# Kernel tuning notes

Hardware: AMD Instinct MI355X
Metric: run time of the kernel (lower is better)

The kernel has to match this reference:

```python
import jax, jax.numpy as jnp
import numpy as np

XY, Zs, V = 32, 16, 10000
N = XY * XY * Zs            # 16384 states
B, T, L = 32, 64, 16
# neighbor offsets from transition_log_p: (x,y,z) -> x + XY*(y + XY*z)
OFFS = np.array([0, 1, -1, XY, -XY, XY * XY, 2 * XY * XY], dtype=np.int64)
NBR = (np.arange(N)[:, None] - OFFS[None, :]) % N   # [N,7] source-state index per neighbor


def setup_inputs() -> dict:
    key = jax.random.key(0)
    k1, k2, k3, k4 = jax.random.split(key, 4)
    return {
        "stories_tensor": jax.random.randint(k1, (B, T, L), 0, V),
        "story_length": T,
        "length": L,
        "trans_unnorm": jax.random.normal(k2, (N, 7), dtype=jnp.float32),
        "emis_unnorm": jax.random.normal(k3, (N, V), dtype=jnp.float32),
        "prior_unnorm": jax.random.normal(k4, (N,), dtype=jnp.float32),
    }


def reference(stories_tensor, story_length, length, trans_unnorm, emis_unnorm, prior_unnorm):
    logT = jax.nn.log_softmax(trans_unnorm, axis=-1)     # [N,7]
    logE = jax.nn.log_softmax(emis_unnorm, axis=1)       # [N,V]
    logpi = jax.nn.log_softmax(prior_unnorm, axis=0)     # [N]
    nbr = jnp.asarray(NBR)                               # [N,7]

    def emit(tokens):                                    # [B,L] -> [B,N]
        # emission_log_p: logE[:, tokens] -> [N,B,L], sum over words, transpose
        return jnp.swapaxes(logE[:, tokens].sum(-1), 0, 1)

    scores0 = emit(stories_tensor[:, 0]) + logpi[None, :]   # [B,N]

    def step(scores, tokens):
        em = emit(tokens)                                # [B,N]
        prev = scores[:, nbr]                            # [B,N,7] gather of prior alpha
        new = em + jax.scipy.special.logsumexp(logT[None, :, :] + prev, axis=-1)
        return new, None

    seq = jnp.swapaxes(stories_tensor, 0, 1)[1:]         # [T-1,B,L]
    scores, _ = jax.lax.scan(step, scores0, seq)
    return jax.scipy.special.logsumexp(scores, axis=-1)  # [B]
```

## Files before the change

kernel.cpp:

```cpp
#include <hip/hip_runtime.h>
#include <stdint.h>

#define XY 32
#define ZS 16
#define NST 16384
#define NMASK 16383
#define VOC 10000
#define BB 32
#define TT 64
#define LL 16
#define HALO 32
#define BUFSZ (NST + 2 * HALO)

#define LOG2E 1.4426950408889634f
#define LN2F  0.6931471805599453f

__device__ __forceinline__ float fexp2(float x) {
#if __has_builtin(__builtin_amdgcn_exp2f)
  return __builtin_amdgcn_exp2f(x);
#else
  return exp2f(x);
#endif
}
__device__ __forceinline__ float flog2(float x) {
#if __has_builtin(__builtin_amdgcn_logf)
  return __builtin_amdgcn_logf(x);
#else
  return log2f(x);
#endif
}

__device__ __forceinline__ float waveMax(float v) {
  #pragma unroll
  for (int o = 32; o >= 1; o >>= 1) v = fmaxf(v, __shfl_xor(v, o, 64));
  return v;
}
__device__ __forceinline__ float waveSum(float v) {
  #pragma unroll
  for (int o = 32; o >= 1; o >>= 1) v += __shfl_xor(v, o, 64);
  return v;
}

__global__ __launch_bounds__(256) void tok_conv(const int* __restrict__ st,
                                                unsigned short* __restrict__ tok16) {
  int i = blockIdx.x * 256 + threadIdx.x;
  if (i >= BB * TT * LL) return;
  int l = i & 15;
  int tb = i >> 4;
  int b = tb & 31;
  int t = tb >> 5;
  tok16[i] = (unsigned short)st[b * (TT * LL) + t * LL + l];
}

__global__ __launch_bounds__(256) void prep_trans(const float* __restrict__ tr,
                                                  float* __restrict__ Tn) {
  int n = blockIdx.x * 256 + threadIdx.x;
  if (n >= NST) return;
  float v[7];
  float m = -3.4e38f;
  #pragma unroll
  for (int k = 0; k < 7; ++k) { v[k] = tr[n * 7 + k]; m = fmaxf(m, v[k]); }
  float s = 0.f;
  #pragma unroll
  for (int k = 0; k < 7; ++k) { v[k] = fexp2((v[k] - m) * LOG2E); s += v[k]; }
  float inv = 1.0f / s;
  #pragma unroll
  for (int k = 0; k < 7; ++k) Tn[n * 8 + k] = v[k] * inv;
  Tn[n * 8 + 7] = 0.f;
}

__global__ __launch_bounds__(256) void lse_prior(const float* __restrict__ prior,
                                                 float* __restrict__ lse_p) {
  int tid = threadIdx.x;
  __shared__ float sred[8];
  float lmax = -3.4e38f;
  for (int n = tid; n < NST; n += 256) lmax = fmaxf(lmax, prior[n]);
  float wm = waveMax(lmax);
  if ((tid & 63) == 0) sred[tid >> 6] = wm;
  __syncthreads();
  float bm = fmaxf(fmaxf(sred[0], sred[1]), fmaxf(sred[2], sred[3]));
  float ls = 0.f;
  for (int n = tid; n < NST; n += 256) ls += fexp2((prior[n] - bm) * LOG2E);
  float ws = waveSum(ls);
  if ((tid & 63) == 0) sred[4 + (tid >> 6)] = ws;
  __syncthreads();
  if (tid == 0)
    lse_p[0] = bm + flog2(sred[4] + sred[5] + sred[6] + sred[7]) * LN2F;
}

__global__ __launch_bounds__(256) void emis_kernel(const float* __restrict__ emis,
                                                   const unsigned short* __restrict__ tok16,
                                                   float* __restrict__ em) {
  const int n = blockIdx.x;
  const int tid = threadIdx.x;
  __shared__ float row[VOC];
  __shared__ float sred[8];

  const float4* rp = (const float4*)(emis + (size_t)n * VOC);
  float4 regs[10];
  float lmax = -3.4e38f;
  #pragma unroll
  for (int it = 0; it < 10; ++it) {
    int i = tid + it * 256;
    if (i < VOC / 4) {
      float4 v = rp[i];
      regs[it] = v;
      ((float4*)row)[i] = v;
      lmax = fmaxf(lmax, fmaxf(fmaxf(v.x, v.y), fmaxf(v.z, v.w)));
    }
  }
  float wm = waveMax(lmax);
  if ((tid & 63) == 0) sred[tid >> 6] = wm;
  __syncthreads();
  float bm = fmaxf(fmaxf(sred[0], sred[1]), fmaxf(sred[2], sred[3]));

  float ls = 0.f;
  #pragma unroll
  for (int it = 0; it < 10; ++it) {
    int i = tid + it * 256;
    if (i < VOC / 4) {
      float4 v = regs[it];
      ls += fexp2((v.x - bm) * LOG2E);
      ls += fexp2((v.y - bm) * LOG2E);
      ls += fexp2((v.z - bm) * LOG2E);
      ls += fexp2((v.w - bm) * LOG2E);
    }
  }
  float wsum = waveSum(ls);
  if ((tid & 63) == 0) sred[4 + (tid >> 6)] = wsum;
  __syncthreads();
  float lse = bm + flog2(sred[4] + sred[5] + sred[6] + sred[7]) * LN2F;
  float sub = (float)LL * lse;

  for (int i = tid; i < TT * BB; i += 256) {
    const uint4* tp = (const uint4*)(tok16 + (size_t)i * 16);
    uint4 w0 = tp[0];
    uint4 w1 = tp[1];
    float s = row[w0.x & 0xFFFF] + row[w0.x >> 16]
            + row[w0.y & 0xFFFF] + row[w0.y >> 16]
            + row[w0.z & 0xFFFF] + row[w0.z >> 16]
            + row[w0.w & 0xFFFF] + row[w0.w >> 16]
            + row[w1.x & 0xFFFF] + row[w1.x >> 16]
            + row[w1.y & 0xFFFF] + row[w1.y >> 16]
            + row[w1.z & 0xFFFF] + row[w1.z >> 16]
            + row[w1.w & 0xFFFF] + row[w1.w >> 16];
    em[(size_t)n * (TT * BB) + i] = (s - sub) * LOG2E;
  }
}

__global__ __launch_bounds__(256) void transpose_em(const float* __restrict__ em,
                                                    float* __restrict__ em2) {
  __shared__ float tile[64][65];
  const int i0 = blockIdx.x * 64;
  const int n0 = blockIdx.y * 64;
  const int tx = threadIdx.x & 63;
  const int ty = threadIdx.x >> 6;
  #pragma unroll
  for (int r = 0; r < 16; ++r) {
    int nr = ty + 4 * r;
    tile[nr][tx] = em[(size_t)(n0 + nr) * (TT * BB) + i0 + tx];
  }
  __syncthreads();
  #pragma unroll
  for (int r = 0; r < 16; ++r) {
    int ir = ty + 4 * r;
    em2[(size_t)(i0 + ir) * NST + n0 + tx] = tile[tx][ir];
  }
}

__global__ __launch_bounds__(1024) void recursion_kernel(const float* __restrict__ em2,
                                                         const float* __restrict__ Tn8,
                                                         const float* __restrict__ prior,
                                                         const float* __restrict__ lse_p,
                                                         float* __restrict__ out) {
  extern __shared__ float lds[];
  float* buf0 = lds;
  float* buf1 = lds + BUFSZ;
  const int b = blockIdx.x;
  const int tid = threadIdx.x;

  {
    const float* e0 = em2 + ((size_t)b << 14);
    #pragma unroll
    for (int s = 0; s < 16; ++s) {
      int n = tid + (s << 10);
      float v = e0[n] + prior[n] * LOG2E;
      buf0[HALO + n] = v;
      if (n < HALO) buf0[HALO + NST + n] = v;
      if (n >= NST - HALO) buf0[n - (NST - HALO)] = v;
    }
  }
  __syncthreads();

  for (int t = 1; t < TT; ++t) {
    const float* prev = (t & 1) ? buf0 : buf1;
    float* cur = (t & 1) ? buf1 : buf0;
    const float* e = em2 + ((size_t)(t * BB + b) << 14);
    float pm1 = prev[HALO + ((tid - 1024) & NMASK)];
    float pm2 = prev[HALO + ((tid - 2048) & NMASK)];
    #pragma unroll
    for (int s = 0; s < 16; ++s) {
      int n = tid + (s << 10);
      float p0 = prev[HALO + n];
      float a1 = prev[HALO + n - 1];
      float a2 = prev[HALO + n + 1];
      float a3 = prev[HALO + n - 32];
      float a4 = prev[HALO + n + 32];
      float p5 = pm1;
      float p6 = pm2;
      const float4* tp = (const float4*)(Tn8 + ((size_t)n << 3));
      float4 ta = tp[0];
      float4 tb = tp[1];
      float m = fmaxf(fmaxf(fmaxf(p0, a1), fmaxf(a2, a3)),
                      fmaxf(fmaxf(a4, p5), p6));
      float ssum = ta.x * fexp2(p0 - m) + ta.y * fexp2(a1 - m)
                 + ta.z * fexp2(a2 - m) + ta.w * fexp2(a3 - m)
                 + tb.x * fexp2(a4 - m) + tb.y * fexp2(p5 - m)
                 + tb.z * fexp2(p6 - m);
      float v = e[n] + m + flog2(ssum);
      cur[HALO + n] = v;
      if (n < HALO) cur[HALO + NST + n] = v;
      if (n >= NST - HALO) cur[n - (NST - HALO)] = v;
      pm2 = pm1;
      pm1 = p0;
    }
    __syncthreads();
  }

  float lm = -3.4e38f;
  #pragma unroll
  for (int s = 0; s < 16; ++s)
    lm = fmaxf(lm, buf1[HALO + tid + (s << 10)]);
  lm = waveMax(lm);
  if ((tid & 63) == 0) buf0[tid >> 6] = lm;
  __syncthreads();
  float bm = buf0[0];
  #pragma unroll
  for (int k = 1; k < 16; ++k) bm = fmaxf(bm, buf0[k]);
  float ls = 0.f;
  #pragma unroll
  for (int s = 0; s < 16; ++s)
    ls += fexp2(buf1[HALO + tid + (s << 10)] - bm);
  ls = waveSum(ls);
  if ((tid & 63) == 0) buf0[16 + (tid >> 6)] = ls;
  __syncthreads();
  if (tid == 0) {
    float s = 0.f;
    #pragma unroll
    for (int k = 0; k < 16; ++k) s += buf0[16 + k];
    out[b] = LN2F * (bm + flog2(s)) - lse_p[0];
  }
}

extern "C" void kernel_launch(void* const* d_in, const int* in_sizes, int n_in,
                              void* d_out, int out_size, void* d_ws, size_t ws_size,
                              hipStream_t stream) {
  const int* stories  = (const int*)d_in[0];
  const float* trans  = (const float*)d_in[3];
  const float* emis   = (const float*)d_in[4];
  const float* prior  = (const float*)d_in[5];
  float* out = (float*)d_out;

  char* ws = (char*)d_ws;
  float* em  = (float*)ws;
  float* em2 = em + (size_t)NST * TT * BB;
  float* Tn  = em2 + (size_t)NST * TT * BB;
  unsigned short* tok16 = (unsigned short*)(Tn + (size_t)NST * 8);
  float* lse_p = (float*)(tok16 + (size_t)BB * TT * LL);

  tok_conv<<<(BB * TT * LL + 255) / 256, 256, 0, stream>>>(stories, tok16);
  prep_trans<<<NST / 256, 256, 0, stream>>>(trans, Tn);
  lse_prior<<<1, 256, 0, stream>>>(prior, lse_p);
  emis_kernel<<<NST, 256, 0, stream>>>(emis, tok16, em);
  transpose_em<<<dim3(TT * BB / 64, NST / 64), 256, 0, stream>>>(em, em2);

  size_t dynlds = (size_t)2 * BUFSZ * sizeof(float);
  hipFuncSetAttribute((const void*)recursion_kernel,
                      hipFuncAttributeMaxDynamicSharedMemorySize, (int)dynlds);
  recursion_kernel<<<BB, 1024, dynlds, stream>>>(em2, Tn, prior, lse_p, out);
}
```

Measured before the change: 1.488 ms.

## Split HMM recursion across 8 chunk blocks per batch with neighbor flag sync

The forward recursion used to run as one 1024-thread block per batch element, which occupies only 32 CUs. It now runs on 256 blocks, each owning a 2048-state chunk of one batch. Each step exchanges state through global double buffers and waits only on per-block flags of the two neighboring chunks, and a final cross-chunk log-sum-exp merges per-chunk partials. Transition weights move to a planar layout cached in LDS. In exchange each step pays a global write, a staged reload of neighbor halos and spin-wait latency, and the scheme depends on all 256 blocks being co-resident to avoid deadlock.

```diff
diff --git a/kernel.cpp b/kernel.cpp
--- a/kernel.cpp
+++ b/kernel.cpp
@@ -9,8 +9,11 @@
 #define BB 32
 #define TT 64
 #define LL 16
-#define HALO 32
-#define BUFSZ (NST + 2 * HALO)
+
+#define NCHUNK 8
+#define CSZ 2048
+#define STAGE_N (CSZ + CSZ + 32)
+#define STAGE_PAD 4160
 
 #define LOG2E 1.4426950408889634f
 #define LN2F  0.6931471805599453f
@@ -53,7 +56,7 @@
 }
 
 __global__ __launch_bounds__(256) void prep_trans(const float* __restrict__ tr,
-                                                  float* __restrict__ Tn) {
+                                                  float* __restrict__ TnG) {
   int n = blockIdx.x * 256 + threadIdx.x;
   if (n >= NST) return;
   float v[7];
@@ -65,8 +68,7 @@
   for (int k = 0; k < 7; ++k) { v[k] = fexp2((v[k] - m) * LOG2E); s += v[k]; }
   float inv = 1.0f / s;
   #pragma unroll
-  for (int k = 0; k < 7; ++k) Tn[n * 8 + k] = v[k] * inv;
-  Tn[n * 8 + 7] = 0.f;
+  for (int k = 0; k < 7; ++k) TnG[k * NST + n] = v[k] * inv;
 }
 
 __global__ __launch_bounds__(256) void lse_prior(const float* __restrict__ prior,
@@ -86,6 +88,10 @@
   __syncthreads();
   if (tid == 0)
     lse_p[0] = bm + flog2(sred[4] + sred[5] + sred[6] + sred[7]) * LN2F;
+}
+
+__global__ __launch_bounds__(64) void init_flags(int* flags) {
+  flags[threadIdx.x + blockIdx.x * 64] = -1;
 }
 
 __global__ __launch_bounds__(256) void emis_kernel(const float* __restrict__ emis,
@@ -168,87 +174,143 @@
   }
 }
 
-__global__ __launch_bounds__(1024) void recursion_kernel(const float* __restrict__ em2,
-                                                         const float* __restrict__ Tn8,
-                                                         const float* __restrict__ prior,
-                                                         const float* __restrict__ lse_p,
-                                                         float* __restrict__ out) {
+__global__ __launch_bounds__(256) void recursion_kernel(
+    const float* __restrict__ em2,
+    const float* __restrict__ TnG,
+    const float* __restrict__ prior,
+    const float* __restrict__ lse_p,
+    float* __restrict__ S0,
+    float* __restrict__ S1,
+    int* flags,
+    float2* partials,
+    float* __restrict__ out) {
   extern __shared__ float lds[];
-  float* buf0 = lds;
-  float* buf1 = lds + BUFSZ;
-  const int b = blockIdx.x;
+  float* stage = lds;
+  float* TnT   = lds + STAGE_PAD;
+  float* red   = TnT + 7 * CSZ;
+
+  const int bid = blockIdx.x;
+  const int b = bid & 31;
+  const int c = bid >> 5;
+  const int c0 = c * CSZ;
   const int tid = threadIdx.x;
-
-  {
-    const float* e0 = em2 + ((size_t)b << 14);
+  const int lbid = (((c + NCHUNK - 1) & (NCHUNK - 1)) << 5) | b;
+  const int rbid = (((c + 1) & (NCHUNK - 1)) << 5) | b;
+
+  #pragma unroll
+  for (int j = 0; j < 7; ++j) {
+    const float4* src = (const float4*)(TnG + (size_t)j * NST + c0);
+    float4* dst = (float4*)(TnT + j * CSZ);
+    for (int i = tid; i < CSZ / 4; i += 256) dst[i] = src[i];
+  }
+
+  #pragma unroll
+  for (int k = 0; k < 8; ++k) {
+    int s = tid + (k << 8);
+    int n = c0 + s;
+    S0[(size_t)b * NST + n] = em2[(size_t)b * NST + n] + prior[n] * LOG2E;
+  }
+  __syncthreads();
+  if (tid == 0)
+    __hip_atomic_store(&flags[bid], 0, __ATOMIC_RELEASE, __HIP_MEMORY_SCOPE_AGENT);
+
+  float vcur[8];
+  for (int t = 1; t < TT; ++t) {
+    const float* __restrict__ Sprev = (t & 1) ? S0 : S1;
+    float* __restrict__ Scur = (t & 1) ? S1 : S0;
+
+    if (tid == 0) {
+      while (__hip_atomic_load(&flags[lbid], __ATOMIC_RELAXED,
+                               __HIP_MEMORY_SCOPE_AGENT) < t - 1)
+        __builtin_amdgcn_s_sleep(1);
+      while (__hip_atomic_load(&flags[rbid], __ATOMIC_RELAXED,
+                               __HIP_MEMORY_SCOPE_AGENT) < t - 1)
+        __builtin_amdgcn_s_sleep(1);
+    }
+    __syncthreads();
+    __builtin_amdgcn_fence(__ATOMIC_ACQUIRE, "agent");
+
+    {
+      const int base = (c0 - CSZ) & NMASK;
+      const float* sp = Sprev + (size_t)b * NST;
+      for (int i = tid; i < STAGE_N / 4; i += 256) {
+        int idx = (base + 4 * i) & NMASK;
+        *(float4*)(stage + 4 * i) = *(const float4*)(sp + idx);
+      }
+    }
+    __syncthreads();
+
+    const float* __restrict__ e = em2 + (size_t)(t * BB + b) * NST + c0;
     #pragma unroll
-    for (int s = 0; s < 16; ++s) {
-      int n = tid + (s << 10);
-      float v = e0[n] + prior[n] * LOG2E;
-      buf0[HALO + n] = v;
-      if (n < HALO) buf0[HALO + NST + n] = v;
-      if (n >= NST - HALO) buf0[n - (NST - HALO)] = v;
-    }
-  }
-  __syncthreads();
-
-  for (int t = 1; t < TT; ++t) {
-    const float* prev = (t & 1) ? buf0 : buf1;
-    float* cur = (t & 1) ? buf1 : buf0;
-    const float* e = em2 + ((size_t)(t * BB + b) << 14);
-    float pm1 = prev[HALO + ((tid - 1024) & NMASK)];
-    float pm2 = prev[HALO + ((tid - 2048) & NMASK)];
-    #pragma unroll
-    for (int s = 0; s < 16; ++s) {
-      int n = tid + (s << 10);
-      float p0 = prev[HALO + n];
-      float a1 = prev[HALO + n - 1];
-      float a2 = prev[HALO + n + 1];
-      float a3 = prev[HALO + n - 32];
-      float a4 = prev[HALO + n + 32];
-      float p5 = pm1;
-      float p6 = pm2;
-      const float4* tp = (const float4*)(Tn8 + ((size_t)n << 3));
-      float4 ta = tp[0];
-      float4 tb = tp[1];
+    for (int k = 0; k < 8; ++k) {
+      int s = tid + (k << 8);
+      float p0 = stage[CSZ + s];
+      float a1 = stage[CSZ + s - 1];
+      float a2 = stage[CSZ + s + 1];
+      float a3 = stage[CSZ + s - 32];
+      float a4 = stage[CSZ + s + 32];
+      float p5 = stage[CSZ + s - 1024];
+      float p6 = stage[s];
+      float t0 = TnT[0 * CSZ + s], t1 = TnT[1 * CSZ + s], t2 = TnT[2 * CSZ + s],
+            t3 = TnT[3 * CSZ + s], t4 = TnT[4 * CSZ + s], t5 = TnT[5 * CSZ + s],
+            t6 = TnT[6 * CSZ + s];
       float m = fmaxf(fmaxf(fmaxf(p0, a1), fmaxf(a2, a3)),
                       fmaxf(fmaxf(a4, p5), p6));
-      float ssum = ta.x * fexp2(p0 - m) + ta.y * fexp2(a1 - m)
-                 + ta.z * fexp2(a2 - m) + ta.w * fexp2(a3 - m)
-                 + tb.x * fexp2(a4 - m) + tb.y * fexp2(p5 - m)
-                 + tb.z * fexp2(p6 - m);
-      float v = e[n] + m + flog2(ssum);
-      cur[HALO + n] = v;
-      if (n < HALO) cur[HALO + NST + n] = v;
-      if (n >= NST - HALO) cur[n - (NST - HALO)] = v;
-      pm2 = pm1;
-      pm1 = p0;
-    }
-    __syncthreads();
-  }
-
-  float lm = -3.4e38f;
-  #pragma unroll
-  for (int s = 0; s < 16; ++s)
-    lm = fmaxf(lm, buf1[HALO + tid + (s << 10)]);
-  lm = waveMax(lm);
-  if ((tid & 63) == 0) buf0[tid >> 6] = lm;
-  __syncthreads();
-  float bm = buf0[0];
-  #pragma unroll
-  for (int k = 1; k < 16; ++k) bm = fmaxf(bm, buf0[k]);
-  float ls = 0.f;
-  #pragma unroll
-  for (int s = 0; s < 16; ++s)
-    ls += fexp2(buf1[HALO + tid + (s << 10)] - bm);
-  ls = waveSum(ls);
-  if ((tid & 63) == 0) buf0[16 + (tid >> 6)] = ls;
+      float ssum = t0 * fexp2(p0 - m) + t1 * fexp2(a1 - m)
+                 + t2 * fexp2(a2 - m) + t3 * fexp2(a3 - m)
+                 + t4 * fexp2(a4 - m) + t5 * fexp2(p5 - m)
+                 + t6 * fexp2(p6 - m);
+      vcur[k] = e[s] + m + flog2(ssum);
+    }
+
+    if (t < TT - 1) {
+      #pragma unroll
+      for (int k = 0; k < 8; ++k)
+        Scur[(size_t)b * NST + c0 + tid + (k << 8)] = vcur[k];
+      __syncthreads();
+      if (tid == 0)
+        __hip_atomic_store(&flags[bid], t, __ATOMIC_RELEASE,
+                           __HIP_MEMORY_SCOPE_AGENT);
+    }
+  }
+
+  float mr = vcur[0];
+  #pragma unroll
+  for (int k = 1; k < 8; ++k) mr = fmaxf(mr, vcur[k]);
+  mr = waveMax(mr);
+  if ((tid & 63) == 0) red[tid >> 6] = mr;
+  __syncthreads();
+  float M = fmaxf(fmaxf(red[0], red[1]), fmaxf(red[2], red[3]));
+  float sr = 0.f;
+  #pragma unroll
+  for (int k = 0; k < 8; ++k) sr += fexp2(vcur[k] - M);
+  sr = waveSum(sr);
+  if ((tid & 63) == 0) red[4 + (tid >> 6)] = sr;
   __syncthreads();
   if (tid == 0) {
-    float s = 0.f;
+    partials[bid] = make_float2(M, red[4] + red[5] + red[6] + red[7]);
+    __hip_atomic_store(&flags[bid], TT - 1, __ATOMIC_RELEASE,
+                       __HIP_MEMORY_SCOPE_AGENT);
+  }
+
+  if (c == 0 && tid == 0) {
     #pragma unroll
-    for (int k = 0; k < 16; ++k) s += buf0[16 + k];
-    out[b] = LN2F * (bm + flog2(s)) - lse_p[0];
+    for (int cc = 1; cc < NCHUNK; ++cc) {
+      int fb = (cc << 5) | b;
+      while (__hip_atomic_load(&flags[fb], __ATOMIC_RELAXED,
+                               __HIP_MEMORY_SCOPE_AGENT) < TT - 1)
+        __builtin_amdgcn_s_sleep(1);
+    }
+    __builtin_amdgcn_fence(__ATOMIC_ACQUIRE, "agent");
+    float Mg = -3.4e38f, Sg = 0.f;
+    #pragma unroll
+    for (int cc = 0; cc < NCHUNK; ++cc) {
+      float2 p = partials[(cc << 5) | b];
+      float nm = fmaxf(Mg, p.x);
+      Sg = Sg * fexp2(Mg - nm) + p.y * fexp2(p.x - nm);
+      Mg = nm;
+    }
+    out[b] = LN2F * (Mg + flog2(Sg)) - lse_p[0];
   }
 }
 
@@ -264,18 +326,24 @@
   char* ws = (char*)d_ws;
   float* em  = (float*)ws;
   float* em2 = em + (size_t)NST * TT * BB;
-  float* Tn  = em2 + (size_t)NST * TT * BB;
-  unsigned short* tok16 = (unsigned short*)(Tn + (size_t)NST * 8);
+  float* S0  = em2 + (size_t)NST * TT * BB;
+  float* S1  = S0 + (size_t)BB * NST;
+  float* TnG = S1 + (size_t)BB * NST;
+  float2* partials = (float2*)(TnG + (size_t)7 * NST);
+  int* flags = (int*)(partials + 256);
+  unsigned short* tok16 = (unsigned short*)(flags + 256);
   float* lse_p = (float*)(tok16 + (size_t)BB * TT * LL);
 
+  init_flags<<<4, 64, 0, stream>>>(flags);
   tok_conv<<<(BB * TT * LL + 255) / 256, 256, 0, stream>>>(stories, tok16);
-  prep_trans<<<NST / 256, 256, 0, stream>>>(trans, Tn);
+  prep_trans<<<NST / 256, 256, 0, stream>>>(trans, TnG);
   lse_prior<<<1, 256, 0, stream>>>(prior, lse_p);
   emis_kernel<<<NST, 256, 0, stream>>>(emis, tok16, em);
   transpose_em<<<dim3(TT * BB / 64, NST / 64), 256, 0, stream>>>(em, em2);
 
-  size_t dynlds = (size_t)2 * BUFSZ * sizeof(float);
+  size_t dynlds = (size_t)(STAGE_PAD + 7 * CSZ + 32) * sizeof(float);
   hipFuncSetAttribute((const void*)recursion_kernel,
                       hipFuncAttributeMaxDynamicSharedMemorySize, (int)dynlds);
-  recursion_kernel<<<BB, 1024, dynlds, stream>>>(em2, Tn, prior, lse_p, out);
-}
+  recursion_kernel<<<BB * NCHUNK, 256, dynlds, stream>>>(
+      em2, TnG, prior, lse_p, S0, S1, flags, partials, out);
+}
```

After: 1.962 ms. 31.8% more time.
